# Kernel tuning notes

Hardware: AMD Instinct MI355X
Metric: run time of the kernel (lower is better)

The kernel has to match this reference:

```python
import jax, jax.numpy as jnp
import numpy as np
from jax import lax

B, T, I = 256, 720, 16   # batch, seq_len, input_dim
H = 128                  # hidden_dim
PRED_LEN = 96


def lstm_cell(x, h, c, W_ih, W_hh, b):
    # PyTorch gate order: i, f, g, o ; b = b_ih + b_hh (combined)
    gates = x @ W_ih.T + h @ W_hh.T + b
    i, f, g, o = jnp.split(gates, 4, axis=-1)
    c = jax.nn.sigmoid(f) * c + jax.nn.sigmoid(i) * jnp.tanh(g)
    h = jax.nn.sigmoid(o) * jnp.tanh(c)
    return h, c


def setup_inputs() -> dict:
    key = jax.random.key(0)
    ks = jax.random.split(key, 16)
    k = 1.0 / np.sqrt(H)
    u = lambda kk, shape: jax.random.uniform(kk, shape, jnp.float32, -k, k)
    inp = {
        "x": jax.random.normal(ks[0], (B, T, I), jnp.float32),
        # encoder (bidirectional, 1 layer): forward + backward directions
        "e_Wih_f": u(ks[1], (4 * H, I)), "e_Whh_f": u(ks[2], (4 * H, H)), "e_b_f": u(ks[3], (4 * H,)),
        "e_Wih_b": u(ks[4], (4 * H, I)), "e_Whh_b": u(ks[5], (4 * H, H)), "e_b_b": u(ks[6], (4 * H,)),
        # decoder (bidirectional, 1 layer)
        "d_Wih_f": u(ks[7], (4 * H, I)), "d_Whh_f": u(ks[8], (4 * H, H)), "d_b_f": u(ks[9], (4 * H,)),
        "d_Wih_b": u(ks[10], (4 * H, I)), "d_Whh_b": u(ks[11], (4 * H, H)), "d_b_b": u(ks[12], (4 * H,)),
        # final linear: (2H -> I)
        "W_lin": u(ks[13], (I, 2 * H)), "b_lin": u(ks[14], (I,)),
    }
    return inp


def reference(x, e_Wih_f, e_Whh_f, e_b_f, e_Wih_b, e_Whh_b, e_b_b,
              d_Wih_f, d_Whh_f, d_b_f, d_Wih_b, d_Whh_b, d_b_b,
              W_lin, b_lin):
    xt = jnp.transpose(x, (1, 0, 2))  # [T, B, I] time-major
    h0 = jnp.zeros((B, H), x.dtype)
    c0 = jnp.zeros((B, H), x.dtype)

    # ---- encoder: bidirectional LSTM; only final (h, c) per direction is used ----
    def enc_f(carry, xt_t):
        h, c = lstm_cell(xt_t, carry[0], carry[1], e_Wih_f, e_Whh_f, e_b_f)
        return (h, c), None

    def enc_b(carry, xt_t):
        h, c = lstm_cell(xt_t, carry[0], carry[1], e_Wih_b, e_Whh_b, e_b_b)
        return (h, c), None

    (hf, cf), _ = lax.scan(enc_f, (h0, c0), xt)
    (hb, cb), _ = lax.scan(enc_b, (h0, c0), xt[::-1])

    def dec_step(carry, _):
        inp, hf, cf, hb, cb = carry
        hf, cf = lstm_cell(inp, hf, cf, d_Wih_f, d_Whh_f, d_b_f)
        hb, cb = lstm_cell(inp, hb, cb, d_Wih_b, d_Whh_b, d_b_b)
        # seq_len==1 so out_f = forward hidden, out_b = backward hidden
        out = jnp.concatenate([hf, hb], axis=-1) @ W_lin.T + b_lin  # [B, I]
        return (out, hf, cf, hb, cb), out

    init = (x[:, -1, :], hf, cf, hb, cb)
    _, outs = lax.scan(dec_step, init, None, length=PRED_LEN)  # [P, B, I]
    return jnp.transpose(outs, (1, 0, 2))  # [B, pred_len, I]
```

## Files before the change

kernel.cpp:

```cpp
#include <hip/hip_runtime.h>
#include <math.h>

#define TB    720
#define NI    16
#define NH    128
#define NG    512
#define PRED  96
#define CHUNK 90

typedef _Float16 h2    __attribute__((ext_vector_type(2)));
typedef _Float16 f16x4 __attribute__((ext_vector_type(4)));
typedef _Float16 f16x8 __attribute__((ext_vector_type(8)));
typedef float    f32x4 __attribute__((ext_vector_type(4)));

__device__ __forceinline__ float rcpf_(float v) {
#if __has_builtin(__builtin_amdgcn_rcpf)
    return __builtin_amdgcn_rcpf(v);
#else
    return 1.0f / v;
#endif
}
__device__ __forceinline__ float sigf(float v)   { return rcpf_(1.0f + __expf(-v)); }
__device__ __forceinline__ float tanhf_(float v) { return 1.0f - 2.0f * rcpf_(1.0f + __expf(2.0f * v)); }

__device__ __forceinline__ unsigned int packf16(float a, float b) {
    h2 p; p.x = (_Float16)a; p.y = (_Float16)b;
    return __builtin_bit_cast(unsigned int, p);
}
__device__ __forceinline__ float2 unpackf16(unsigned int u) {
    h2 p = __builtin_bit_cast(h2, u);
    return make_float2((float)p.x, (float)p.y);
}
__device__ __forceinline__ float fdot2f(unsigned int a, unsigned int b, float c) {
#if __has_builtin(__builtin_amdgcn_fdot2)
    return __builtin_amdgcn_fdot2(__builtin_bit_cast(h2, a), __builtin_bit_cast(h2, b), c, false);
#else
    h2 x = __builtin_bit_cast(h2, a), y = __builtin_bit_cast(h2, b);
    return c + (float)x.x * (float)y.x + (float)x.y * (float)y.y;
#endif
}

__device__ __forceinline__ f16x8 mk8(const float* p) {
    f16x8 v;
    v[0] = (_Float16)p[0];  v[1] = (_Float16)p[1];  v[2] = (_Float16)p[2];  v[3] = (_Float16)p[3];
    v[4] = (_Float16)p[16]; v[5] = (_Float16)p[17]; v[6] = (_Float16)p[18]; v[7] = (_Float16)p[19];
    return v;
}
__device__ __forceinline__ f32x4 MFMA(f16x8 a, f16x8 b, f32x4 c) {
    return __builtin_amdgcn_mfma_f32_16x16x32_f16(a, b, c, 0, 0, 0);
}

__global__ __launch_bounds__(512, 1)
void enc_kernel(const float* __restrict__ x,
                const float* __restrict__ Wih_f, const float* __restrict__ Whh_f, const float* __restrict__ b_f,
                const float* __restrict__ Wih_b, const float* __restrict__ Whh_b, const float* __restrict__ b_b,
                float* __restrict__ st)
{
    __shared__ _Float16 hbuf0[16 * NH];
    __shared__ _Float16 hbuf1[16 * NH];
    __shared__ unsigned int xsh[CHUNK * 128];

    const int blk = blockIdx.x;
    const int dir = blk & 1;
    const int b0  = (blk >> 1) << 4;
    const int t   = threadIdx.x;
    const int wv  = t >> 6;
    const int l   = t & 63;
    const int lr  = l & 15;
    const int lk  = l >> 4;

    const float* Wih = dir ? Wih_b : Wih_f;
    const float* Whh = dir ? Whh_b : Whh_f;
    const float* bv  = dir ? b_b   : b_f;

    const int mt0 = wv * 4, mt1 = wv * 4 + 1, mt2 = wv * 4 + 2, mt3 = wv * 4 + 3;
    const int R0 = mt0 * 16 + lr, R1 = mt1 * 16 + lr, R2 = mt2 * 16 + lr, R3 = mt3 * 16 + lr;
    const int or0 = (R0 & 3) * 128 + (R0 >> 2);
    const int or1 = (R1 & 3) * 128 + (R1 >> 2);
    const int or2 = (R2 & 3) * 128 + (R2 >> 2);
    const int or3 = (R3 & 3) * 128 + (R3 >> 2);
    const float* p0 = Whh + (size_t)or0 * NH + lk * 4;
    const float* p1 = Whh + (size_t)or1 * NH + lk * 4;
    const float* p2 = Whh + (size_t)or2 * NH + lk * 4;
    const float* p3 = Whh + (size_t)or3 * NH + lk * 4;
    f16x8 w0_0 = mk8(p0), w0_1 = mk8(p0 + 32), w0_2 = mk8(p0 + 64), w0_3 = mk8(p0 + 96);
    f16x8 w1_0 = mk8(p1), w1_1 = mk8(p1 + 32), w1_2 = mk8(p1 + 64), w1_3 = mk8(p1 + 96);
    f16x8 w2_0 = mk8(p2), w2_1 = mk8(p2 + 32), w2_2 = mk8(p2 + 64), w2_3 = mk8(p2 + 96);
    f16x8 w3_0 = mk8(p3), w3_1 = mk8(p3 + 32), w3_2 = mk8(p3 + 64), w3_3 = mk8(p3 + 96);

    f16x8 ax0, ax1, ax2, ax3;
#define MKAXR(DST, OR) { \
    const float* xr_ = Wih + (size_t)(OR) * NI + lk * 4; \
    DST[0] = (_Float16)xr_[0]; DST[1] = (_Float16)xr_[1]; \
    DST[2] = (_Float16)xr_[2]; DST[3] = (_Float16)xr_[3]; \
    DST[4] = (_Float16)bv[(OR)]; \
    DST[5] = (_Float16)0.f; DST[6] = (_Float16)0.f; DST[7] = (_Float16)0.f; }
    MKAXR(ax0, or0) MKAXR(ax1, or1) MKAXR(ax2, or2) MKAXR(ax3, or3)
#undef MKAXR

    const int d0 = mt0 * 4 + lk, d1 = mt1 * 4 + lk, d2 = mt2 * 4 + lk, d3 = mt3 * 4 + lk;

    ((unsigned int*)hbuf0)[t] = 0u;
    ((unsigned int*)hbuf0)[t + 512] = 0u;
    float cs0 = 0.f, cs1 = 0.f, cs2 = 0.f, cs3 = 0.f;

    const int hro0 = 0 * 1024 + lk * 256 + lr * 16;
    const int hro1 = 1 * 1024 + lk * 256 + lr * 16;
    const int hro2 = 2 * 1024 + lk * 256 + lr * 16;
    const int hro3 = 3 * 1024 + lk * 256 + lr * 16;
#define CWB(D) ((((D) >> 5) * 1024) + ((((D) & 15) >> 2) * 256) + lr * 16 + (((((D) & 31) >> 4) * 4 + ((D) & 3)) * 2))
    const int cwb0 = CWB(d0), cwb1 = CWB(d1), cwb2 = CWB(d2), cwb3 = CWB(d3);
#undef CWB
    const int xoff = lk * 128 + lr * 8;
    f16x8 bxT;
    bxT[0] = (_Float16)0.f; bxT[1] = (_Float16)0.f; bxT[2] = (_Float16)0.f; bxT[3] = (_Float16)0.f;
    bxT[4] = (lk == 0) ? (_Float16)1.0f : (_Float16)0.f;
    bxT[5] = (_Float16)0.f; bxT[6] = (_Float16)0.f; bxT[7] = (_Float16)0.f;
    const f32x4 CZ = {0.f, 0.f, 0.f, 0.f};
    __syncthreads();

#define CELL(J, HW) { \
    float ci_ = sigf(C##J[0]), cf_ = sigf(C##J[1]); \
    float cg_ = tanhf_(C##J[2]), co_ = sigf(C##J[3]); \
    cs##J = cf_ * cs##J + ci_ * cg_; \
    float hv_ = co_ * tanhf_(cs##J); \
    *(_Float16*)((char*)(HW) + cwb##J) = (_Float16)hv_; }

#define STEP(HR, HW, SI) { \
    const char* hrb_ = (const char*)(HR); \
    f16x8 bh0 = *(const f16x8*)(hrb_ + hro0); \
    f16x8 bh1 = *(const f16x8*)(hrb_ + hro1); \
    f16x8 bh2 = *(const f16x8*)(hrb_ + hro2); \
    f16x8 bh3 = *(const f16x8*)(hrb_ + hro3); \
    f16x8 bx = bxT; \
    *(f16x4*)&bx = *(const f16x4*)((const char*)xsh + (SI) * 512 + xoff); \
    f32x4 C0 = MFMA(ax0, bx, CZ); f32x4 C1 = MFMA(ax1, bx, CZ); \
    f32x4 C2 = MFMA(ax2, bx, CZ); f32x4 C3 = MFMA(ax3, bx, CZ); \
    C0 = MFMA(w0_0, bh0, C0); C1 = MFMA(w1_0, bh0, C1); \
    C2 = MFMA(w2_0, bh0, C2); C3 = MFMA(w3_0, bh0, C3); \
    C0 = MFMA(w0_1, bh1, C0); C1 = MFMA(w1_1, bh1, C1); \
    C2 = MFMA(w2_1, bh1, C2); C3 = MFMA(w3_1, bh1, C3); \
    C0 = MFMA(w0_2, bh2, C0); C1 = MFMA(w1_2, bh2, C1); \
    C2 = MFMA(w2_2, bh2, C2); C3 = MFMA(w3_2, bh2, C3); \
    C0 = MFMA(w0_3, bh3, C0); C1 = MFMA(w1_3, bh3, C1); \
    C2 = MFMA(w2_3, bh3, C2); C3 = MFMA(w3_3, bh3, C3); \
    CELL(0, HW) CELL(1, HW) CELL(2, HW) CELL(3, HW) \
    __syncthreads(); }

    for (int c = 0; c < 8; ++c) {
        {
            const int c0 = c * CHUNK;
            for (int i = t; i < 16 * CHUNK * 8; i += 512) {
                const int br  = i / (CHUNK * 8);
                const int rem = i - br * (CHUNK * 8);
                const int ti  = rem >> 3;
                const int dw  = rem & 7;
                const int s_  = c0 + ti;
                const int tt  = dir ? (TB - 1 - s_) : s_;
                float2 v = *(const float2*)(x + ((size_t)(b0 + br) * TB + tt) * NI + dw * 2);
                xsh[ti * 128 + (dw >> 1) * 32 + br * 2 + (dw & 1)] = packf16(v.x, v.y);
            }
        }
        __syncthreads();
        for (int si2 = 0; si2 < CHUNK / 2; ++si2) {
            STEP(hbuf0, hbuf1, si2 * 2)
            STEP(hbuf1, hbuf0, si2 * 2 + 1)
        }
    }
#undef STEP
#undef CELL

    {
        const size_t base = ((size_t)(b0 + lr) * 2 + dir) * 2 * NH;
#define FIN(J) { \
        float hv_ = (float)*(const _Float16*)((const char*)hbuf0 + cwb##J); \
        st[base + d##J] = hv_; st[base + NH + d##J] = cs##J; }
        FIN(0) FIN(1) FIN(2) FIN(3)
#undef FIN
    }
}

#define R8(F)  F(0)F(1)F(2)F(3)F(4)F(5)F(6)F(7)
#define R36_(F) F(8)F(9)F(10)F(11)F(12)F(13)F(14)F(15)F(16)F(17)F(18)F(19)F(20)F(21)F(22)F(23)F(24)F(25)F(26)F(27)F(28)F(29)F(30)F(31)F(32)F(33)F(34)F(35)
#define R36(F) R8(F) R36_(F)
#define R64(F) R36(F) F(36)F(37)F(38)F(39)F(40)F(41)F(42)F(43)F(44)F(45)F(46)F(47)F(48)F(49)F(50)F(51)F(52)F(53)F(54)F(55)F(56)F(57)F(58)F(59)F(60)F(61)F(62)F(63)

#define QD(Q,i0,i1,i2,i3) { a0 = fdot2f((Q).x, w##i0, a0); a1 = fdot2f((Q).y, w##i1, a1); \
                            a2 = fdot2f((Q).z, w##i2, a2); a3 = fdot2f((Q).w, w##i3, a3); }
#define QDU(Q,i0,i1,i2,i3) { a0 = fdot2f((Q).x, u##i0, a0); a1 = fdot2f((Q).y, u##i1, a1); \
                             a2 = fdot2f((Q).z, u##i2, a2); a3 = fdot2f((Q).w, u##i3, a3); }

__global__ __launch_bounds__(1024, 1)
void dec_kernel(const float* __restrict__ x,
                const float* __restrict__ Wih_f, const float* __restrict__ Whh_f, const float* __restrict__ b_f,
                const float* __restrict__ Wih_b, const float* __restrict__ Whh_b, const float* __restrict__ b_b,
                const float* __restrict__ Wlin, const float* __restrict__ blin,
                const float* __restrict__ st, float* __restrict__ out)
{
    __shared__ unsigned int hFh[NH / 2], hBh[NH / 2];
    __shared__ unsigned int inpH[NI / 2];
    __shared__ float g[1024];
    __shared__ float prt[NG];
    __shared__ float wlin_s[16 * 256];
    __shared__ float blin_s[16];
    __shared__ float obuf[PRED * 16];

    const int b    = blockIdx.x;
    const int t    = threadIdx.x;
    const int cell = t >> 9;
    const int r    = t & 511;

    const float* Wih = cell ? Wih_b : Wih_f;
    const float* Whh = cell ? Whh_b : Whh_f;
    const float* bv  = cell ? b_b   : b_f;

    for (int i = t; i < 16 * 256; i += 1024) wlin_s[i] = Wlin[i];
    if (t < 16) blin_s[t] = blin[t];

#define DW(K) unsigned int w##K;
    R64(DW)
#undef DW
#define DU(K) unsigned int u##K;
    R8(DU)
#undef DU
    {
        const float* xr = Wih + r * NI;
        const float* hr = Whh + r * NH;
#define LU(K) u##K = packf16(xr[2*(K)], xr[2*(K)+1]);
        R8(LU)
#undef LU
#define LH(K) w##K = packf16(hr[2*(K)], hr[2*(K)+1]);
        R64(LH)
#undef LH
    }
    const float bias = bv[r];

    float cc = 0.0f;
    if (t < 64) {
        const float* sh = st + ((b * 2 + 0) * 2 + 0) * NH;
        hFh[t] = packf16(sh[2 * t], sh[2 * t + 1]);
    } else if (t < 128) {
        const float* sh = st + ((b * 2 + 1) * 2 + 0) * NH;
        hBh[t - 64] = packf16(sh[2 * (t - 64)], sh[2 * (t - 64) + 1]);
    }
    if (t < NH) cc = st[((b * 2 + 0) * 2 + 1) * NH + t];
    else if (t >= 512 && t < 512 + NH) cc = st[((b * 2 + 1) * 2 + 1) * NH + (t - 512)];
    if (t < 8) {
        float2 v = ((const float2*)(x + (size_t)b * TB * NI + (TB - 1) * NI))[t];
        inpH[t] = packf16(v.x, v.y);
    }
    __syncthreads();

    for (int s = 0; s < PRED; ++s) {
        float a0 = bias, a1 = 0.f, a2 = 0.f, a3 = 0.f;
        uint4 q;
        {
            const uint4* xv = (const uint4*)inpH;
            q = xv[0]; QDU(q, 0, 1, 2, 3)
            q = xv[1]; QDU(q, 4, 5, 6, 7)
        }
        const uint4* hv = cell ? (const uint4*)hBh : (const uint4*)hFh;
        q = hv[0];  QD(q, 0, 1, 2, 3)
        q = hv[1];  QD(q, 4, 5, 6, 7)
        q = hv[2];  QD(q, 8, 9, 10, 11)
        q = hv[3];  QD(q, 12, 13, 14, 15)
        q = hv[4];  QD(q, 16, 17, 18, 19)
        q = hv[5];  QD(q, 20, 21, 22, 23)
        q = hv[6];  QD(q, 24, 25, 26, 27)
        q = hv[7];  QD(q, 28, 29, 30, 31)
        q = hv[8];  QD(q, 32, 33, 34, 35)
        q = hv[9];  QD(q, 36, 37, 38, 39)
        q = hv[10]; QD(q, 40, 41, 42, 43)
        q = hv[11]; QD(q, 44, 45, 46, 47)
        q = hv[12]; QD(q, 48, 49, 50, 51)
        q = hv[13]; QD(q, 52, 53, 54, 55)
        q = hv[14]; QD(q, 56, 57, 58, 59)
        q = hv[15]; QD(q, 60, 61, 62, 63)
        g[t] = (a0 + a1) + (a2 + a3);
        __syncthreads();
        if ((t < NH) || (t >= 512 && t < 512 + NH)) {
            float gi = g[t], gf = g[t + NH], gg = g[t + 2 * NH], go = g[t + 3 * NH];
            cc = sigf(gf) * cc + sigf(gi) * tanhf_(gg);
            float h = sigf(go) * tanhf_(cc);
            if (t < NH) ((_Float16*)hFh)[t] = (_Float16)h;
            else        ((_Float16*)hBh)[t - 512] = (_Float16)h;
        }
        __syncthreads();
        if (t < NG) {
            const int j = t >> 5, ch = t & 31;
            const unsigned int* hsrc = (ch < 16) ? (hFh + ch * 4) : (hBh + (ch - 16) * 4);
            const float* wl = wlin_s + j * 256 + ch * 8;
            float2 v0 = unpackf16(hsrc[0]);
            float2 v1 = unpackf16(hsrc[1]);
            float2 v2 = unpackf16(hsrc[2]);
            float2 v3 = unpackf16(hsrc[3]);
            prt[t] = v0.x * wl[0] + v0.y * wl[1] + v1.x * wl[2] + v1.y * wl[3]
                   + v2.x * wl[4] + v2.y * wl[5] + v3.x * wl[6] + v3.y * wl[7];
        }
        __syncthreads();
        if (t < NI) {
            float o = blin_s[t];
#pragma unroll
            for (int c2 = 0; c2 < 32; ++c2) o += prt[t * 32 + c2];
            obuf[s * NI + t] = o;
            ((_Float16*)inpH)[t] = (_Float16)o;
        }
        __syncthreads();
    }

    {
        float4* dst = (float4*)(out + (size_t)b * PRED * NI);
        const float4* src = (const float4*)obuf;
        for (int i = t; i < PRED * NI / 4; i += 1024) dst[i] = src[i];
    }
}

extern "C" void kernel_launch(void* const* d_in, const int* in_sizes, int n_in,
                              void* d_out, int out_size, void* d_ws, size_t ws_size,
                              hipStream_t stream)
{
    const float* x      = (const float*)d_in[0];
    const float* eWih_f = (const float*)d_in[1];
    const float* eWhh_f = (const float*)d_in[2];
    const float* eb_f   = (const float*)d_in[3];
    const float* eWih_b = (const float*)d_in[4];
    const float* eWhh_b = (const float*)d_in[5];
    const float* eb_b   = (const float*)d_in[6];
    const float* dWih_f = (const float*)d_in[7];
    const float* dWhh_f = (const float*)d_in[8];
    const float* db_f   = (const float*)d_in[9];
    const float* dWih_b = (const float*)d_in[10];
    const float* dWhh_b = (const float*)d_in[11];
    const float* db_b   = (const float*)d_in[12];
    const float* Wlin   = (const float*)d_in[13];
    const float* blin   = (const float*)d_in[14];

    float* st = (float*)d_ws;

    enc_kernel<<<32, 512, 0, stream>>>(x, eWih_f, eWhh_f, eb_f, eWih_b, eWhh_b, eb_b, st);
    dec_kernel<<<256, 1024, 0, stream>>>(x, dWih_f, dWhh_f, db_f, dWih_b, dWhh_b, db_b,
                                         Wlin, blin, st, (float*)d_out);
}
```

Baseline: 853.3 us.

## Fold log2e into encoder weights, shrink decoder register weights, fuse output linear

The encoder pre-scales gate weights and biases by log2(e) (2*log2(e) for the g gate) so the cell can use raw exp2. It also shares one reciprocal between each pair of gates to cut transcendental work on the serial recurrence path. The decoder keeps only 36 of 64 packed recurrent weight registers per thread and moves the rest, plus the input weights, into LDS. This lowers register pressure at 1024 threads. The output linear becomes a per-wave shuffle reduction written straight to global memory, dropping one barrier per step and the staging buffer, at the cost of extra LDS reads and fp16 rounding of the pre-scaled weights.

```diff
diff --git a/kernel.cpp b/kernel.cpp
--- a/kernel.cpp
+++ b/kernel.cpp
@@ -13,11 +13,21 @@
 typedef _Float16 f16x8 __attribute__((ext_vector_type(8)));
 typedef float    f32x4 __attribute__((ext_vector_type(4)));
 
+#define LOG2E  1.4426950408889634f
+#define LOG2E2 2.8853900817779268f
+
 __device__ __forceinline__ float rcpf_(float v) {
 #if __has_builtin(__builtin_amdgcn_rcpf)
     return __builtin_amdgcn_rcpf(v);
 #else
     return 1.0f / v;
+#endif
+}
+__device__ __forceinline__ float ex2(float v) {
+#if __has_builtin(__builtin_amdgcn_exp2f)
+    return __builtin_amdgcn_exp2f(v);
+#else
+    return exp2f(v);
 #endif
 }
 __device__ __forceinline__ float sigf(float v)   { return rcpf_(1.0f + __expf(-v)); }
@@ -40,10 +50,12 @@
 #endif
 }
 
-__device__ __forceinline__ f16x8 mk8(const float* p) {
+__device__ __forceinline__ f16x8 mk8s(const float* p, float s) {
     f16x8 v;
-    v[0] = (_Float16)p[0];  v[1] = (_Float16)p[1];  v[2] = (_Float16)p[2];  v[3] = (_Float16)p[3];
-    v[4] = (_Float16)p[16]; v[5] = (_Float16)p[17]; v[6] = (_Float16)p[18]; v[7] = (_Float16)p[19];
+    v[0] = (_Float16)(p[0]  * s); v[1] = (_Float16)(p[1]  * s);
+    v[2] = (_Float16)(p[2]  * s); v[3] = (_Float16)(p[3]  * s);
+    v[4] = (_Float16)(p[16] * s); v[5] = (_Float16)(p[17] * s);
+    v[6] = (_Float16)(p[18] * s); v[7] = (_Float16)(p[19] * s);
     return v;
 }
 __device__ __forceinline__ f32x4 MFMA(f16x8 a, f16x8 b, f32x4 c) {
@@ -79,23 +91,27 @@
     const int or1 = (R1 & 3) * 128 + (R1 >> 2);
     const int or2 = (R2 & 3) * 128 + (R2 >> 2);
     const int or3 = (R3 & 3) * 128 + (R3 >> 2);
+    const float s0 = ((or0 >> 7) == 2) ? LOG2E2 : LOG2E;
+    const float s1 = ((or1 >> 7) == 2) ? LOG2E2 : LOG2E;
+    const float s2 = ((or2 >> 7) == 2) ? LOG2E2 : LOG2E;
+    const float s3 = ((or3 >> 7) == 2) ? LOG2E2 : LOG2E;
     const float* p0 = Whh + (size_t)or0 * NH + lk * 4;
     const float* p1 = Whh + (size_t)or1 * NH + lk * 4;
     const float* p2 = Whh + (size_t)or2 * NH + lk * 4;
     const float* p3 = Whh + (size_t)or3 * NH + lk * 4;
-    f16x8 w0_0 = mk8(p0), w0_1 = mk8(p0 + 32), w0_2 = mk8(p0 + 64), w0_3 = mk8(p0 + 96);
-    f16x8 w1_0 = mk8(p1), w1_1 = mk8(p1 + 32), w1_2 = mk8(p1 + 64), w1_3 = mk8(p1 + 96);
-    f16x8 w2_0 = mk8(p2), w2_1 = mk8(p2 + 32), w2_2 = mk8(p2 + 64), w2_3 = mk8(p2 + 96);
-    f16x8 w3_0 = mk8(p3), w3_1 = mk8(p3 + 32), w3_2 = mk8(p3 + 64), w3_3 = mk8(p3 + 96);
+    f16x8 w0_0 = mk8s(p0, s0), w0_1 = mk8s(p0 + 32, s0), w0_2 = mk8s(p0 + 64, s0), w0_3 = mk8s(p0 + 96, s0);
+    f16x8 w1_0 = mk8s(p1, s1), w1_1 = mk8s(p1 + 32, s1), w1_2 = mk8s(p1 + 64, s1), w1_3 = mk8s(p1 + 96, s1);
+    f16x8 w2_0 = mk8s(p2, s2), w2_1 = mk8s(p2 + 32, s2), w2_2 = mk8s(p2 + 64, s2), w2_3 = mk8s(p2 + 96, s2);
+    f16x8 w3_0 = mk8s(p3, s3), w3_1 = mk8s(p3 + 32, s3), w3_2 = mk8s(p3 + 64, s3), w3_3 = mk8s(p3 + 96, s3);
 
     f16x8 ax0, ax1, ax2, ax3;
-#define MKAXR(DST, OR) { \
+#define MKAXR(DST, OR, SC) { \
     const float* xr_ = Wih + (size_t)(OR) * NI + lk * 4; \
-    DST[0] = (_Float16)xr_[0]; DST[1] = (_Float16)xr_[1]; \
-    DST[2] = (_Float16)xr_[2]; DST[3] = (_Float16)xr_[3]; \
-    DST[4] = (_Float16)bv[(OR)]; \
+    DST[0] = (_Float16)(xr_[0] * (SC)); DST[1] = (_Float16)(xr_[1] * (SC)); \
+    DST[2] = (_Float16)(xr_[2] * (SC)); DST[3] = (_Float16)(xr_[3] * (SC)); \
+    DST[4] = (_Float16)(bv[(OR)] * (SC)); \
     DST[5] = (_Float16)0.f; DST[6] = (_Float16)0.f; DST[7] = (_Float16)0.f; }
-    MKAXR(ax0, or0) MKAXR(ax1, or1) MKAXR(ax2, or2) MKAXR(ax3, or3)
+    MKAXR(ax0, or0, s0) MKAXR(ax1, or1, s1) MKAXR(ax2, or2, s2) MKAXR(ax3, or3, s3)
 #undef MKAXR
 
     const int d0 = mt0 * 4 + lk, d1 = mt1 * 4 + lk, d2 = mt2 * 4 + lk, d3 = mt3 * 4 + lk;
@@ -120,10 +136,16 @@
     __syncthreads();
 
 #define CELL(J, HW) { \
-    float ci_ = sigf(C##J[0]), cf_ = sigf(C##J[1]); \
-    float cg_ = tanhf_(C##J[2]), co_ = sigf(C##J[3]); \
-    cs##J = cf_ * cs##J + ci_ * cg_; \
-    float hv_ = co_ * tanhf_(cs##J); \
+    float ei_ = ex2(-C##J[0]), ef_ = ex2(-C##J[1]); \
+    float eg_ = ex2(C##J[2]),  eo_ = ex2(-C##J[3]); \
+    float di_ = 1.f + ei_, df_ = 1.f + ef_, dg_ = 1.f + eg_, dq_ = 1.f + eo_; \
+    float r1_ = rcpf_(di_ * df_), r2_ = rcpf_(dq_ * dg_); \
+    float si_ = r1_ * df_, sf_ = r1_ * di_, so_ = r2_ * dg_; \
+    float tg_ = __builtin_fmaf(-2.f * r2_, dq_, 1.f); \
+    cs##J = sf_ * cs##J + si_ * tg_; \
+    float ec_ = ex2(cs##J * LOG2E2); \
+    float th_ = __builtin_fmaf(-2.f, rcpf_(1.f + ec_), 1.f); \
+    float hv_ = so_ * th_; \
     *(_Float16*)((char*)(HW) + cwb##J) = (_Float16)hv_; }
 
 #define STEP(HR, HW, SI) { \
@@ -183,12 +205,11 @@
 #define R8(F)  F(0)F(1)F(2)F(3)F(4)F(5)F(6)F(7)
 #define R36_(F) F(8)F(9)F(10)F(11)F(12)F(13)F(14)F(15)F(16)F(17)F(18)F(19)F(20)F(21)F(22)F(23)F(24)F(25)F(26)F(27)F(28)F(29)F(30)F(31)F(32)F(33)F(34)F(35)
 #define R36(F) R8(F) R36_(F)
-#define R64(F) R36(F) F(36)F(37)F(38)F(39)F(40)F(41)F(42)F(43)F(44)F(45)F(46)F(47)F(48)F(49)F(50)F(51)F(52)F(53)F(54)F(55)F(56)F(57)F(58)F(59)F(60)F(61)F(62)F(63)
 
 #define QD(Q,i0,i1,i2,i3) { a0 = fdot2f((Q).x, w##i0, a0); a1 = fdot2f((Q).y, w##i1, a1); \
                             a2 = fdot2f((Q).z, w##i2, a2); a3 = fdot2f((Q).w, w##i3, a3); }
-#define QDU(Q,i0,i1,i2,i3) { a0 = fdot2f((Q).x, u##i0, a0); a1 = fdot2f((Q).y, u##i1, a1); \
-                             a2 = fdot2f((Q).z, u##i2, a2); a3 = fdot2f((Q).w, u##i3, a3); }
+#define QDS(HQ, SQ) { a0 = fdot2f((HQ).x, (SQ).x, a0); a1 = fdot2f((HQ).y, (SQ).y, a1); \
+                      a2 = fdot2f((HQ).z, (SQ).z, a2); a3 = fdot2f((HQ).w, (SQ).w, a3); }
 
 __global__ __launch_bounds__(1024, 1)
 void dec_kernel(const float* __restrict__ x,
@@ -200,40 +221,51 @@
     __shared__ unsigned int hFh[NH / 2], hBh[NH / 2];
     __shared__ unsigned int inpH[NI / 2];
     __shared__ float g[1024];
-    __shared__ float prt[NG];
-    __shared__ float wlin_s[16 * 256];
-    __shared__ float blin_s[16];
-    __shared__ float obuf[PRED * 16];
+    __shared__ uint4 ws[9 * 1024];
 
     const int b    = blockIdx.x;
     const int t    = threadIdx.x;
     const int cell = t >> 9;
     const int r    = t & 511;
+    const int w    = t >> 6;
+    const int ln   = t & 63;
 
     const float* Wih = cell ? Wih_b : Wih_f;
     const float* Whh = cell ? Whh_b : Whh_f;
     const float* bv  = cell ? b_b   : b_f;
 
-    for (int i = t; i < 16 * 256; i += 1024) wlin_s[i] = Wlin[i];
-    if (t < 16) blin_s[t] = blin[t];
-
 #define DW(K) unsigned int w##K;
-    R64(DW)
+    R36(DW)
 #undef DW
-#define DU(K) unsigned int u##K;
-    R8(DU)
-#undef DU
     {
+        const float* hr = Whh + r * NH;
+#define LH(K) w##K = packf16(hr[2*(K)], hr[2*(K)+1]);
+        R36(LH)
+#undef LH
         const float* xr = Wih + r * NI;
-        const float* hr = Whh + r * NH;
-#define LU(K) u##K = packf16(xr[2*(K)], xr[2*(K)+1]);
-        R8(LU)
-#undef LU
-#define LH(K) w##K = packf16(hr[2*(K)], hr[2*(K)+1]);
-        R64(LH)
-#undef LH
+#pragma unroll
+        for (int kk = 0; kk < 7; ++kk) {
+            const float* pp = hr + 72 + kk * 8;
+            uint4 q;
+            q.x = packf16(pp[0], pp[1]); q.y = packf16(pp[2], pp[3]);
+            q.z = packf16(pp[4], pp[5]); q.w = packf16(pp[6], pp[7]);
+            ws[kk * 1024 + t] = q;
+        }
+        uint4 qa, qb;
+        qa.x = packf16(xr[0], xr[1]);   qa.y = packf16(xr[2], xr[3]);
+        qa.z = packf16(xr[4], xr[5]);   qa.w = packf16(xr[6], xr[7]);
+        qb.x = packf16(xr[8], xr[9]);   qb.y = packf16(xr[10], xr[11]);
+        qb.z = packf16(xr[12], xr[13]); qb.w = packf16(xr[14], xr[15]);
+        ws[7 * 1024 + t] = qa;
+        ws[8 * 1024 + t] = qb;
     }
     const float bias = bv[r];
+
+    const float wl0 = Wlin[w * 256 + ln * 4 + 0];
+    const float wl1 = Wlin[w * 256 + ln * 4 + 1];
+    const float wl2 = Wlin[w * 256 + ln * 4 + 2];
+    const float wl3 = Wlin[w * 256 + ln * 4 + 3];
+    const float blw = blin[w];
 
     float cc = 0.0f;
     if (t < 64) {
@@ -254,30 +286,26 @@
     for (int s = 0; s < PRED; ++s) {
         float a0 = bias, a1 = 0.f, a2 = 0.f, a3 = 0.f;
         uint4 q;
+        const uint4* hv = cell ? (const uint4*)hBh : (const uint4*)hFh;
+        q = hv[0]; QD(q, 0, 1, 2, 3)
+        q = hv[1]; QD(q, 4, 5, 6, 7)
+        q = hv[2]; QD(q, 8, 9, 10, 11)
+        q = hv[3]; QD(q, 12, 13, 14, 15)
+        q = hv[4]; QD(q, 16, 17, 18, 19)
+        q = hv[5]; QD(q, 20, 21, 22, 23)
+        q = hv[6]; QD(q, 24, 25, 26, 27)
+        q = hv[7]; QD(q, 28, 29, 30, 31)
+        q = hv[8]; QD(q, 32, 33, 34, 35)
+#pragma unroll
+        for (int kk = 0; kk < 7; ++kk) { QDS(hv[9 + kk], ws[kk * 1024 + t]) }
         {
             const uint4* xv = (const uint4*)inpH;
-            q = xv[0]; QDU(q, 0, 1, 2, 3)
-            q = xv[1]; QDU(q, 4, 5, 6, 7)
-        }
-        const uint4* hv = cell ? (const uint4*)hBh : (const uint4*)hFh;
-        q = hv[0];  QD(q, 0, 1, 2, 3)
-        q = hv[1];  QD(q, 4, 5, 6, 7)
-        q = hv[2];  QD(q, 8, 9, 10, 11)
-        q = hv[3];  QD(q, 12, 13, 14, 15)
-        q = hv[4];  QD(q, 16, 17, 18, 19)
-        q = hv[5];  QD(q, 20, 21, 22, 23)
-        q = hv[6];  QD(q, 24, 25, 26, 27)
-        q = hv[7];  QD(q, 28, 29, 30, 31)
-        q = hv[8];  QD(q, 32, 33, 34, 35)
-        q = hv[9];  QD(q, 36, 37, 38, 39)
-        q = hv[10]; QD(q, 40, 41, 42, 43)
-        q = hv[11]; QD(q, 44, 45, 46, 47)
-        q = hv[12]; QD(q, 48, 49, 50, 51)
-        q = hv[13]; QD(q, 52, 53, 54, 55)
-        q = hv[14]; QD(q, 56, 57, 58, 59)
-        q = hv[15]; QD(q, 60, 61, 62, 63)
+            QDS(xv[0], ws[7 * 1024 + t])
+            QDS(xv[1], ws[8 * 1024 + t])
+        }
         g[t] = (a0 + a1) + (a2 + a3);
         __syncthreads();
+
         if ((t < NH) || (t >= 512 && t < 512 + NH)) {
             float gi = g[t], gf = g[t + NH], gg = g[t + 2 * NH], go = g[t + 3 * NH];
             cc = sigf(gf) * cc + sigf(gi) * tanhf_(gg);
@@ -286,32 +314,21 @@
             else        ((_Float16*)hBh)[t - 512] = (_Float16)h;
         }
         __syncthreads();
-        if (t < NG) {
-            const int j = t >> 5, ch = t & 31;
-            const unsigned int* hsrc = (ch < 16) ? (hFh + ch * 4) : (hBh + (ch - 16) * 4);
-            const float* wl = wlin_s + j * 256 + ch * 8;
-            float2 v0 = unpackf16(hsrc[0]);
-            float2 v1 = unpackf16(hsrc[1]);
-            float2 v2 = unpackf16(hsrc[2]);
-            float2 v3 = unpackf16(hsrc[3]);
-            prt[t] = v0.x * wl[0] + v0.y * wl[1] + v1.x * wl[2] + v1.y * wl[3]
-                   + v2.x * wl[4] + v2.y * wl[5] + v3.x * wl[6] + v3.y * wl[7];
+
+        {
+            const unsigned int* hsrc = (ln < 32) ? (hFh + 2 * ln) : (hBh + 2 * (ln - 32));
+            uint2 hw = *(const uint2*)hsrc;
+            float2 va = unpackf16(hw.x), vb = unpackf16(hw.y);
+            float p = va.x * wl0 + va.y * wl1 + vb.x * wl2 + vb.y * wl3;
+            p += __shfl_xor(p, 1);  p += __shfl_xor(p, 2);  p += __shfl_xor(p, 4);
+            p += __shfl_xor(p, 8);  p += __shfl_xor(p, 16); p += __shfl_xor(p, 32);
+            if (ln == 0) {
+                float o = p + blw;
+                out[(size_t)b * PRED * NI + s * NI + w] = o;
+                ((_Float16*)inpH)[w] = (_Float16)o;
+            }
         }
         __syncthreads();
-        if (t < NI) {
-            float o = blin_s[t];
-#pragma unroll
-            for (int c2 = 0; c2 < 32; ++c2) o += prt[t * 32 + c2];
-            obuf[s * NI + t] = o;
-            ((_Float16*)inpH)[t] = (_Float16)o;
-        }
-        __syncthreads();
-    }
-
-    {
-        float4* dst = (float4*)(out + (size_t)b * PRED * NI);
-        const float4* src = (const float4*)obuf;
-        for (int i = t; i < PRED * NI / 4; i += 1024) dst[i] = src[i];
     }
 }
 
```

After: 861.2 us. About the same (+0.9%).
